# Performance work log

Measured on AMD Instinct MI355X. Metric: run time of the kernel, lower is better.

Reference implementation:

```python
import jax, jax.numpy as jnp
import numpy as np

H = 8          # attention heads
DV = 32        # per-head dim for view2global (256/8)
DS = 32        # per-head dim for scenepoint2global (256/8)
DG = 512       # n_feat_global_out
DIN = 256      # n_feat_view_in == n_feat_scenepoint_in
EPS = 1e-5


def layernorm(x, scale, bias):
    m = jnp.mean(x, axis=-1, keepdims=True)
    v = jnp.var(x, axis=-1, keepdims=True)
    return (x - m) / jnp.sqrt(v + EPS) * scale + bias


def gatv2_star(x_src, x_tgt, Wl, bl, Wr, br, att, out_bias, heads, dim):
    """GATv2Conv over a star graph: every source node -> single target node.
    x_src: [N, Din], x_tgt: [1, Din]. Returns [1, heads*dim]."""
    xl = (x_src @ Wl + bl).reshape(-1, heads, dim)          # [N,H,D] messages
    xr = (x_tgt @ Wr + br).reshape(1, heads, dim)           # [1,H,D]
    e = jax.nn.leaky_relu(xl + xr, negative_slope=0.2)      # [N,H,D]
    logits = jnp.einsum('nhd,hd->nh', e, att)               # [N,H]
    alpha = jax.nn.softmax(logits, axis=0)                  # softmax over edges per head
    out = jnp.einsum('nh,nhd->hd', alpha, xl).reshape(1, heads * dim)
    return out + out_bias


def setup_inputs() -> dict:
    key = jax.random.key(0)
    ks = jax.random.split(key, 24)
    s = 0.05
    inp = {
        'view_features': jax.random.normal(ks[0], (4096, DIN), jnp.float32),
        'scenepoint_features': jax.random.normal(ks[1], (262144, DIN), jnp.float32),
        'prev_global_features': jax.random.normal(ks[2], (1, DG), jnp.float32),
        # norm_and_proj_global2view: LayerNorm(512) -> ReLU -> Linear(512,256)
        'g2v_ln_s': jnp.ones((DG,), jnp.float32),
        'g2v_ln_b': jnp.zeros((DG,), jnp.float32),
        'g2v_W': jax.random.normal(ks[3], (DG, DIN), jnp.float32) * s,
        'g2v_b': jnp.zeros((DIN,), jnp.float32),
        # norm_and_proj_global2scenepoint
        'g2s_ln_s': jnp.ones((DG,), jnp.float32),
        'g2s_ln_b': jnp.zeros((DG,), jnp.float32),
        'g2s_W': jax.random.normal(ks[4], (DG, DIN), jnp.float32) * s,
        'g2s_b': jnp.zeros((DIN,), jnp.float32),
        # GATv2Conv view2global
        'v_Wl': jax.random.normal(ks[5], (DIN, H * DV), jnp.float32) * s,
        'v_bl': jnp.zeros((H * DV,), jnp.float32),
        'v_Wr': jax.random.normal(ks[6], (DIN, H * DV), jnp.float32) * s,
        'v_br': jnp.zeros((H * DV,), jnp.float32),
        'v_att': jax.random.normal(ks[7], (H, DV), jnp.float32) * s,
        'v_bias': jnp.zeros((H * DV,), jnp.float32),
        # GATv2Conv scenepoint2global
        's_Wl': jax.random.normal(ks[8], (DIN, H * DS), jnp.float32) * s,
        's_bl': jnp.zeros((H * DS,), jnp.float32),
        's_Wr': jax.random.normal(ks[9], (DIN, H * DS), jnp.float32) * s,
        's_br': jnp.zeros((H * DS,), jnp.float32),
        's_att': jax.random.normal(ks[10], (H, DS), jnp.float32) * s,
        's_bias': jnp.zeros((H * DS,), jnp.float32),
        # norm_pre_mlp + mlp (single Linear 512->512, no norm inside mlp)
        'pre_ln_s': jnp.ones((DG,), jnp.float32),
        'pre_ln_b': jnp.zeros((DG,), jnp.float32),
        'mlp_W': jax.random.normal(ks[11], (DG, DG), jnp.float32) * s,
        'mlp_b': jnp.zeros((DG,), jnp.float32),
    }
    return inp


def reference(view_features, scenepoint_features, prev_global_features,
              g2v_ln_s, g2v_ln_b, g2v_W, g2v_b,
              g2s_ln_s, g2s_ln_b, g2s_W, g2s_b,
              v_Wl, v_bl, v_Wr, v_br, v_att, v_bias,
              s_Wl, s_bl, s_Wr, s_br, s_att, s_bias,
              pre_ln_s, pre_ln_b, mlp_W, mlp_b):
    # target-node input features for each star graph
    xt_v = jax.nn.relu(layernorm(prev_global_features, g2v_ln_s, g2v_ln_b)) @ g2v_W + g2v_b
    xt_s = jax.nn.relu(layernorm(prev_global_features, g2s_ln_s, g2s_ln_b)) @ g2s_W + g2s_b
    v2g = gatv2_star(view_features, xt_v, v_Wl, v_bl, v_Wr, v_br, v_att, v_bias, H, DV)
    s2g = gatv2_star(scenepoint_features, xt_s, s_Wl, s_bl, s_Wr, s_br, s_att, s_bias, H, DS)
    x = jnp.concatenate([v2g, s2g], axis=1)                 # [1, 512] == n_feat_global_out
    x = prev_global_features + x                            # stateful residual
    x_skip = x
    x = jax.nn.relu(layernorm(x, pre_ln_s, pre_ln_b))       # norm_pre_mlp + relu
    x = x @ mlp_W + mlp_b                                   # mlp (0 hidden layers)
    return x_skip + x
```

## Files before the change

### kernel.cpp

```cpp
#include <hip/hip_runtime.h>
#include <hip/hip_bf16.h>

typedef unsigned short ushort_t;
typedef __attribute__((ext_vector_type(8))) short bf16x8;
typedef __attribute__((ext_vector_type(4))) float f32x4;

#define NBS 480
#define NBV 32
#define SLDS 264

#define WS_XR    0
#define WS_ACC   512
#define WS_SKIP  1040
#define WS_XN    1552

__device__ __forceinline__ float bf2f(ushort_t u) {
    union { unsigned int i; float f; } v; v.i = ((unsigned int)u) << 16; return v.f;
}
__device__ __forceinline__ ushort_t f2bf(float f) {
    union { float f; unsigned int i; } v; v.f = f;
    unsigned int x = v.i;
    return (ushort_t)((x + 0x7fffu + ((x >> 16) & 1u)) >> 16);
}
template<bool F32>
__device__ __forceinline__ float ldT(const void* p, int i) {
    if (F32) return ((const float*)p)[i];
    return bf2f(((const ushort_t*)p)[i]);
}
__device__ __forceinline__ bool is_bf16(const void* det) {
    return ((const ushort_t*)det)[0] == 0x3F80u;
}

__device__ __forceinline__ float qsum16(float x) {
    union { float f; int i; } a, b;
#define QS_STEP(CTRL) { a.f = x; b.i = __builtin_amdgcn_update_dpp(0, a.i, CTRL, 0xF, 0xF, true); x += b.f; }
    QS_STEP(0x128)
    QS_STEP(0x124)
    QS_STEP(0x122)
    QS_STEP(0x121)
#undef QS_STEP
    return x;
}

template<bool F32>
__global__ __launch_bounds__(512)
void prep_k(const void* __restrict__ prev,
            const void* __restrict__ lns_v, const void* __restrict__ lnb_v,
            const void* __restrict__ W_v,   const void* __restrict__ b_v,
            const void* __restrict__ Wr_v,  const void* __restrict__ br_v,
            const void* __restrict__ lns_s, const void* __restrict__ lnb_s,
            const void* __restrict__ W_s,   const void* __restrict__ b_s,
            const void* __restrict__ Wr_s,  const void* __restrict__ br_s,
            float* __restrict__ xr, float* __restrict__ accSO)
{
    if (is_bf16(lns_v) == F32) return;
    const int br = blockIdx.x;
    const void* lns = br ? lns_s : lns_v;
    const void* lnb = br ? lnb_s : lnb_v;
    const void* W   = br ? W_s   : W_v;
    const void* bb  = br ? b_s   : b_v;
    const void* Wr  = br ? Wr_s  : Wr_v;
    const void* brr = br ? br_s  : br_v;
    const int t = threadIdx.x;
    for (int i = t; i < 264; i += 512) accSO[br*264 + i] = 0.f;

    __shared__ float g[512];
    __shared__ float xt[256];
    __shared__ float red[16];
    __shared__ float stats[2];
    __shared__ float part[512];

    float a0 = ldT<F32>(prev, t);
    float s1 = a0, s2 = a0*a0;
#pragma unroll
    for (int s = 1; s < 64; s <<= 1) { s1 += __shfl_xor(s1, s); s2 += __shfl_xor(s2, s); }
    if ((t & 63) == 0) { red[t >> 6] = s1; red[8 + (t >> 6)] = s2; }
    __syncthreads();
    if (t == 0) {
        float a = 0.f, q = 0.f;
        for (int i = 0; i < 8; i++) { a += red[i]; q += red[8 + i]; }
        float mean = a / 512.f;
        stats[0] = mean;
        stats[1] = rsqrtf(q / 512.f - mean*mean + 1e-5f);
    }
    __syncthreads();
    g[t] = fmaxf((a0 - stats[0])*stats[1]*ldT<F32>(lns, t) + ldT<F32>(lnb, t), 0.f);
    __syncthreads();

    const int c = t & 255, kh = t >> 8;
    {
        const int base = kh * 256;
        float acc = 0.f;
#pragma unroll 8
        for (int i = 0; i < 256; i++) acc += g[base + i] * ldT<F32>(W, (base + i)*256 + c);
        part[t] = acc;
    }
    __syncthreads();
    if (t < 256) xt[t] = part[t] + part[t + 256] + ldT<F32>(bb, t);
    __syncthreads();

    {
        const int b2 = kh * 128;
        float acc2 = 0.f;
#pragma unroll 8
        for (int j = 0; j < 128; j++) acc2 += xt[b2 + j] * ldT<F32>(Wr, (b2 + j)*256 + c);
        part[t] = acc2;
    }
    __syncthreads();
    if (t < 256) xr[br*256 + t] = part[t] + part[t + 256] + ldT<F32>(brr, t);
}

template<bool F32>
__global__ __launch_bounds__(512, 2)
void gat_k(const void* __restrict__ view_x, const void* __restrict__ scene_x,
           const void* __restrict__ v_Wl, const void* __restrict__ s_Wl,
           const float* __restrict__ xr_all,
           const void* __restrict__ v_bl, const void* __restrict__ s_bl,
           const void* __restrict__ v_att, const void* __restrict__ s_att,
           const void* __restrict__ det,
           float* __restrict__ accSO)
{
    if (is_bf16(det) == F32) return;

    const int tid = threadIdx.x;
    const int wave = tid >> 6;
    const int lane = tid & 63;
    const int quad = lane >> 4;
    const int li   = lane & 15;

    const int bid = blockIdx.x;
    const bool scene = bid < NBS;
    const void* xsrc = scene ? scene_x : view_x;
    const void* Wl   = scene ? s_Wl : v_Wl;
    const float* xrp = xr_all + (scene ? 256 : 0);
    const void* blp  = scene ? s_bl  : v_bl;
    const void* attp = scene ? s_att : v_att;
    float* accR      = accSO + (scene ? 264 : 0);
    const int ntiles = scene ? 4096 : 64;
    const int nb     = scene ? NBS : NBV;
    const int slot   = scene ? bid : (bid - NBS);

    bf16x8 Bf[2][8];
#pragma unroll
    for (int nt = 0; nt < 2; nt++)
#pragma unroll
        for (int k = 0; k < 8; k++) {
            union { ushort_t u[8]; bf16x8 v; } tmp;
#pragma unroll
            for (int j = 0; j < 8; j++) {
                int idx = (k*32 + quad*8 + j)*256 + (wave*32 + nt*16 + li);
                tmp.u[j] = F32 ? f2bf(((const float*)Wl)[idx]) : ((const ushort_t*)Wl)[idx];
            }
            Bf[nt][k] = tmp.v;
        }

    const int c0 = wave*32 + li;
    const float xr0 = xrp[c0],             xr1 = xrp[c0 + 16];
    const float at0 = ldT<F32>(attp, c0),  at1 = ldT<F32>(attp, c0 + 16);
    const float bl0 = ldT<F32>(blp, c0),   bl1 = ldT<F32>(blp, c0 + 16);

    float Ssum = 0.f, oa0 = 0.f, oa1 = 0.f;

    __shared__ __align__(16) ushort_t alds[2][64 * SLDS];

    auto stage = [&](int tile, int i) -> int4 {
        int f = tid + 512*i;
        int row = f >> 5, c8 = f & 31;
        size_t base = (size_t)(tile*64 + row)*256 + c8*8;
        if (F32) {
            const float* p = (const float*)xsrc + base;
            float4 a = *(const float4*)p, b = *(const float4*)(p + 4);
            union { ushort_t u[8]; int4 v; } t_;
            t_.u[0]=f2bf(a.x); t_.u[1]=f2bf(a.y); t_.u[2]=f2bf(a.z); t_.u[3]=f2bf(a.w);
            t_.u[4]=f2bf(b.x); t_.u[5]=f2bf(b.y); t_.u[6]=f2bf(b.z); t_.u[7]=f2bf(b.w);
            return t_.v;
        }
        return *(const int4*)((const ushort_t*)xsrc + base);
    };
    auto ldsw = [&](int b, int4* src) {
#pragma unroll
        for (int i = 0; i < 4; i++) {
            int f = tid + 512*i;
            int row = f >> 5, c8 = f & 31;
            *(int4*)(&alds[b][row*SLDS + c8*8]) = src[i];
        }
    };

    int4 pf[2][4];
    {
        int4 t0[4];
#pragma unroll
        for (int i = 0; i < 4; i++) t0[i] = stage(slot, i);
        ldsw(0, t0);
        if (slot + nb < ntiles) {
#pragma unroll
            for (int i = 0; i < 4; i++) pf[0][i] = stage(slot + nb, i);
        }
        if (slot + 2*nb < ntiles) {
#pragma unroll
            for (int i = 0; i < 4; i++) pf[1][i] = stage(slot + 2*nb, i);
        }
        __syncthreads();
    }

    int buf = 0, par = 0;
    for (int t = slot; t < ntiles; t += nb) {
        f32x4 acc[4][2] = {};
#pragma unroll
        for (int k = 0; k < 8; k++) {
            bf16x8 a[4];
#pragma unroll
            for (int m = 0; m < 4; m++)
                a[m] = *(const bf16x8*)(&alds[buf][(m*16 + li)*SLDS + k*32 + quad*8]);
#pragma unroll
            for (int m = 0; m < 4; m++) {
                acc[m][0] = __builtin_amdgcn_mfma_f32_16x16x32_bf16(a[m], Bf[0][k], acc[m][0], 0, 0, 0);
                acc[m][1] = __builtin_amdgcn_mfma_f32_16x16x32_bf16(a[m], Bf[1][k], acc[m][1], 0, 0, 0);
            }
        }

#pragma unroll
        for (int m = 0; m < 4; m++) {
#pragma unroll
            for (int r = 0; r < 4; r++) {
                float x0 = acc[m][0][r] + bl0;
                float x1 = acc[m][1][r] + bl1;
                float e0 = x0 + xr0; e0 = e0 > 0.f ? e0 : 0.2f*e0;
                float e1 = x1 + xr1; e1 = e1 > 0.f ? e1 : 0.2f*e1;
                float p = qsum16(at0*e0 + at1*e1);
                float w = __expf(fminf(p, 60.f));
                Ssum += w;
                oa0 += w * x0;
                oa1 += w * x1;
            }
        }

        if (t + nb < ntiles) {
            ldsw(buf ^ 1, pf[par]);
            int tf = t + 3*nb;
            if (tf < ntiles) {
#pragma unroll
                for (int i = 0; i < 4; i++) pf[par][i] = stage(tf, i);
            }
        }
        __syncthreads();
        buf ^= 1; par ^= 1;
    }

    Ssum += __shfl_xor(Ssum, 16); Ssum += __shfl_xor(Ssum, 32);
    oa0  += __shfl_xor(oa0, 16);  oa0  += __shfl_xor(oa0, 32);
    oa1  += __shfl_xor(oa1, 16);  oa1  += __shfl_xor(oa1, 32);

    if (lane == 0) atomicAdd(&accR[wave], Ssum);
    if (lane < 16) {
        atomicAdd(&accR[8 + wave*32 + lane],      oa0);
        atomicAdd(&accR[8 + wave*32 + 16 + lane], oa1);
    }
}

template<bool F32>
__global__ __launch_bounds__(512)
void combine_k(const float* __restrict__ accSO,
               const void* __restrict__ prev,
               const void* __restrict__ v_bias, const void* __restrict__ s_bias,
               const void* __restrict__ pre_s, const void* __restrict__ pre_b,
               const void* __restrict__ det,
               float* __restrict__ x_skip, float* __restrict__ xn)
{
    if (is_bf16(det) == F32) return;
    const int t = threadIdx.x;
    const int branch = t >> 8, c = t & 255, h = c >> 5;
    float S = accSO[branch*264 + h];
    float o = accSO[branch*264 + 8 + c];
    const void* bias = branch ? s_bias : v_bias;
    float xv = ldT<F32>(prev, t) + o / S + ldT<F32>(bias, c);
    x_skip[t] = xv;
    __shared__ float red[16];
    __shared__ float stats[2];
    float s1 = xv, s2 = xv*xv;
#pragma unroll
    for (int s = 1; s < 64; s <<= 1) { s1 += __shfl_xor(s1, s); s2 += __shfl_xor(s2, s); }
    if ((t & 63) == 0) { red[t >> 6] = s1; red[8 + (t >> 6)] = s2; }
    __syncthreads();
    if (t == 0) {
        float a = 0.f, q = 0.f;
        for (int i = 0; i < 8; i++) { a += red[i]; q += red[8 + i]; }
        float mean = a / 512.f;
        stats[0] = mean;
        stats[1] = rsqrtf(q / 512.f - mean*mean + 1e-5f);
    }
    __syncthreads();
    float xnv = (xv - stats[0]) * stats[1] * ldT<F32>(pre_s, t) + ldT<F32>(pre_b, t);
    xn[t] = fmaxf(xnv, 0.f);
}

template<bool F32>
__global__ __launch_bounds__(256)
void mlp_k(const float* __restrict__ x_skip, const float* __restrict__ xn,
           const void* __restrict__ W, const void* __restrict__ mb,
           const void* __restrict__ det,
           void* __restrict__ out)
{
    if (is_bf16(det) == F32) return;
    __shared__ float xs[512];
    __shared__ float part[256];
    const int t = threadIdx.x;
    for (int i = t; i < 512; i += 256) xs[i] = xn[i];
    __syncthreads();
    const int c = blockIdx.x*128 + (t & 127);
    const int kh = t >> 7;
    const int b = kh * 256;
    float acc = 0.f;
#pragma unroll 8
    for (int i = 0; i < 256; i++) acc += xs[b + i] * ldT<F32>(W, (b + i)*512 + c);
    part[t] = acc;
    __syncthreads();
    if (t < 128) {
        float r = x_skip[c] + part[t] + part[t + 128] + ldT<F32>(mb, c);
        if (F32) ((float*)out)[c] = r;
        else     ((ushort_t*)out)[c] = f2bf(r);
    }
}

extern "C" void kernel_launch(void* const* d_in, const int* in_sizes, int n_in,
                              void* d_out, int out_size, void* d_ws, size_t ws_size,
                              hipStream_t stream)
{
    const void* view_x  = d_in[0];
    const void* scene_x = d_in[1];
    const void* prev    = d_in[2];
    const void* g2v_lns = d_in[3];
    const void* g2v_lnb = d_in[4];
    const void* g2v_W   = d_in[5];
    const void* g2v_b   = d_in[6];
    const void* g2s_lns = d_in[7];
    const void* g2s_lnb = d_in[8];
    const void* g2s_W   = d_in[9];
    const void* g2s_b   = d_in[10];
    const void* v_Wl    = d_in[11];
    const void* v_bl    = d_in[12];
    const void* v_Wr    = d_in[13];
    const void* v_br    = d_in[14];
    const void* v_att   = d_in[15];
    const void* v_bias  = d_in[16];
    const void* s_Wl    = d_in[17];
    const void* s_bl    = d_in[18];
    const void* s_Wr    = d_in[19];
    const void* s_br    = d_in[20];
    const void* s_att   = d_in[21];
    const void* s_bias  = d_in[22];
    const void* pre_s   = d_in[23];
    const void* pre_b   = d_in[24];
    const void* mlp_W   = d_in[25];
    const void* mlp_b   = d_in[26];

    float* wsf    = (float*)d_ws;
    float* xr     = wsf + WS_XR;
    float* accSO  = wsf + WS_ACC;
    float* x_skip = wsf + WS_SKIP;
    float* xn     = wsf + WS_XN;

    prep_k<false><<<dim3(2), dim3(512), 0, stream>>>(prev,
                                              g2v_lns, g2v_lnb, g2v_W, g2v_b, v_Wr, v_br,
                                              g2s_lns, g2s_lnb, g2s_W, g2s_b, s_Wr, s_br,
                                              xr, accSO);
    prep_k<true><<<dim3(2), dim3(512), 0, stream>>>(prev,
                                              g2v_lns, g2v_lnb, g2v_W, g2v_b, v_Wr, v_br,
                                              g2s_lns, g2s_lnb, g2s_W, g2s_b, s_Wr, s_br,
                                              xr, accSO);
    gat_k<false><<<dim3(NBS + NBV), dim3(512), 0, stream>>>(view_x, scene_x, v_Wl, s_Wl, xr,
                                                            v_bl, s_bl, v_att, s_att,
                                                            g2v_lns, accSO);
    gat_k<true><<<dim3(NBS + NBV), dim3(512), 0, stream>>>(view_x, scene_x, v_Wl, s_Wl, xr,
                                                           v_bl, s_bl, v_att, s_att,
                                                           g2v_lns, accSO);
    combine_k<false><<<dim3(1), dim3(512), 0, stream>>>(accSO, prev, v_bias, s_bias,
                                                        pre_s, pre_b, g2v_lns, x_skip, xn);
    combine_k<true><<<dim3(1), dim3(512), 0, stream>>>(accSO, prev, v_bias, s_bias,
                                                       pre_s, pre_b, g2v_lns, x_skip, xn);
    mlp_k<false><<<dim3(4), dim3(256), 0, stream>>>(x_skip, xn, mlp_W, mlp_b, g2v_lns, d_out);
    mlp_k<true><<<dim3(4), dim3(256), 0, stream>>>(x_skip, xn, mlp_W, mlp_b, g2v_lns, d_out);
}
```

Before: 562.5 us.

## Launch one block per tile with async LDS loads and bucketed atomics

Replaces the persistent grid-stride GAT kernel (512 blocks looping over tiles with register-prefetch double buffering) with one block per 64-row tile. In bf16 mode tiles are loaded straight into XOR-swizzled LDS using global_load_lds. Accumulation atomics are spread across 16 bucket copies to reduce contention, and combine sums the buckets. The small prep and mlp GEMVs batch 32 weight loads before accumulating, and mlp uses more blocks. The cost is that every block now reloads the full 256x256 Wl weight fragment into registers, and there are many more block launches and atomics.

```diff
diff --git a/kernel.cpp b/kernel.cpp
--- a/kernel.cpp
+++ b/kernel.cpp
@@ -5,14 +5,14 @@
 typedef __attribute__((ext_vector_type(8))) short bf16x8;
 typedef __attribute__((ext_vector_type(4))) float f32x4;
 
-#define NBS 480
-#define NBV 32
-#define SLDS 264
+#define NSCENE 4096
+#define NVIEW  64
+#define NBUCK  16
 
 #define WS_XR    0
 #define WS_ACC   512
-#define WS_SKIP  1040
-#define WS_XN    1552
+#define WS_SKIP  (512 + NBUCK*528)
+#define WS_XN    (WS_SKIP + 512)
 
 __device__ __forceinline__ float bf2f(ushort_t u) {
     union { unsigned int i; float f; } v; v.i = ((unsigned int)u) << 16; return v.f;
@@ -30,7 +30,11 @@
 __device__ __forceinline__ bool is_bf16(const void* det) {
     return ((const ushort_t*)det)[0] == 0x3F80u;
 }
-
+__device__ __forceinline__ void async16(const void* g, void* lds) {
+    __builtin_amdgcn_global_load_lds(
+        (const __attribute__((address_space(1))) unsigned int*)g,
+        (__attribute__((address_space(3))) unsigned int*)lds, 16, 0, 0);
+}
 __device__ __forceinline__ float qsum16(float x) {
     union { float f; int i; } a, b;
 #define QS_STEP(CTRL) { a.f = x; b.i = __builtin_amdgcn_update_dpp(0, a.i, CTRL, 0xF, 0xF, true); x += b.f; }
@@ -62,7 +66,9 @@
     const void* Wr  = br ? Wr_s  : Wr_v;
     const void* brr = br ? br_s  : br_v;
     const int t = threadIdx.x;
-    for (int i = t; i < 264; i += 512) accSO[br*264 + i] = 0.f;
+#pragma unroll
+    for (int b = 0; b < NBUCK; b++)
+        for (int i = t; i < 264; i += 512) accSO[b*528 + br*264 + i] = 0.f;
 
     __shared__ float g[512];
     __shared__ float xt[256];
@@ -91,19 +97,28 @@
     {
         const int base = kh * 256;
         float acc = 0.f;
-#pragma unroll 8
-        for (int i = 0; i < 256; i++) acc += g[base + i] * ldT<F32>(W, (base + i)*256 + c);
+        for (int ii = 0; ii < 256; ii += 32) {
+            float wv[32];
+#pragma unroll
+            for (int u = 0; u < 32; u++) wv[u] = ldT<F32>(W, (base + ii + u)*256 + c);
+#pragma unroll
+            for (int u = 0; u < 32; u++) acc += g[base + ii + u] * wv[u];
+        }
         part[t] = acc;
     }
     __syncthreads();
     if (t < 256) xt[t] = part[t] + part[t + 256] + ldT<F32>(bb, t);
     __syncthreads();
-
     {
         const int b2 = kh * 128;
         float acc2 = 0.f;
-#pragma unroll 8
-        for (int j = 0; j < 128; j++) acc2 += xt[b2 + j] * ldT<F32>(Wr, (b2 + j)*256 + c);
+        for (int ii = 0; ii < 128; ii += 32) {
+            float wv[32];
+#pragma unroll
+            for (int u = 0; u < 32; u++) wv[u] = ldT<F32>(Wr, (b2 + ii + u)*256 + c);
+#pragma unroll
+            for (int u = 0; u < 32; u++) acc2 += xt[b2 + ii + u] * wv[u];
+        }
         part[t] = acc2;
     }
     __syncthreads();
@@ -122,23 +137,44 @@
 {
     if (is_bf16(det) == F32) return;
 
-    const int tid = threadIdx.x;
+    const int tid  = threadIdx.x;
     const int wave = tid >> 6;
     const int lane = tid & 63;
     const int quad = lane >> 4;
     const int li   = lane & 15;
 
-    const int bid = blockIdx.x;
-    const bool scene = bid < NBS;
+    const int bid   = blockIdx.x;
+    const bool scene = bid < NSCENE;
     const void* xsrc = scene ? scene_x : view_x;
     const void* Wl   = scene ? s_Wl : v_Wl;
     const float* xrp = xr_all + (scene ? 256 : 0);
     const void* blp  = scene ? s_bl  : v_bl;
     const void* attp = scene ? s_att : v_att;
-    float* accR      = accSO + (scene ? 264 : 0);
-    const int ntiles = scene ? 4096 : 64;
-    const int nb     = scene ? NBS : NBV;
-    const int slot   = scene ? bid : (bid - NBS);
+    float* accR      = accSO + (bid & (NBUCK - 1))*528 + (scene ? 264 : 0);
+    const int tile   = scene ? bid : (bid - NSCENE);
+
+    __shared__ __align__(16) ushort_t alds[64 * 256];
+
+    {
+        const int l5 = lane >> 5, g2 = lane & 31;
+#pragma unroll
+        for (int j = 0; j < 4; j++) {
+            const int ci  = wave*4 + j;
+            const int row = 2*ci + l5;
+            const int g   = (g2 & 24) | ((g2 & 7) ^ (row & 7));
+            const size_t gelem = (size_t)(tile*64 + row)*256 + g*8;
+            if (F32) {
+                const float* p = (const float*)xsrc + gelem;
+                float4 a = *(const float4*)p, b = *(const float4*)(p + 4);
+                union { ushort_t u[8]; int4 v; } t_;
+                t_.u[0]=f2bf(a.x); t_.u[1]=f2bf(a.y); t_.u[2]=f2bf(a.z); t_.u[3]=f2bf(a.w);
+                t_.u[4]=f2bf(b.x); t_.u[5]=f2bf(b.y); t_.u[6]=f2bf(b.z); t_.u[7]=f2bf(b.w);
+                *(int4*)(&alds[ci*512 + lane*8]) = t_.v;
+            } else {
+                async16((const ushort_t*)xsrc + gelem, &alds[ci*512]);
+            }
+        }
+    }
 
     bf16x8 Bf[2][8];
 #pragma unroll
@@ -155,96 +191,45 @@
         }
 
     const int c0 = wave*32 + li;
-    const float xr0 = xrp[c0],             xr1 = xrp[c0 + 16];
-    const float at0 = ldT<F32>(attp, c0),  at1 = ldT<F32>(attp, c0 + 16);
-    const float bl0 = ldT<F32>(blp, c0),   bl1 = ldT<F32>(blp, c0 + 16);
+    const float xr0 = xrp[c0],            xr1 = xrp[c0 + 16];
+    const float at0 = ldT<F32>(attp, c0), at1 = ldT<F32>(attp, c0 + 16);
+    const float bl0 = ldT<F32>(blp, c0),  bl1 = ldT<F32>(blp, c0 + 16);
+
+    __syncthreads();
+
+    f32x4 acc[4][2] = {};
+#pragma unroll
+    for (int k = 0; k < 8; k++) {
+        bf16x8 a[4];
+#pragma unroll
+        for (int m = 0; m < 4; m++) {
+            const int r  = m*16 + li;
+            const int gq = k*4 + quad;
+            const int gp = (gq & 24) | ((gq & 7) ^ (li & 7));
+            a[m] = *(const bf16x8*)(&alds[r*256 + gp*8]);
+        }
+#pragma unroll
+        for (int m = 0; m < 4; m++) {
+            acc[m][0] = __builtin_amdgcn_mfma_f32_16x16x32_bf16(a[m], Bf[0][k], acc[m][0], 0, 0, 0);
+            acc[m][1] = __builtin_amdgcn_mfma_f32_16x16x32_bf16(a[m], Bf[1][k], acc[m][1], 0, 0, 0);
+        }
+    }
 
     float Ssum = 0.f, oa0 = 0.f, oa1 = 0.f;
-
-    __shared__ __align__(16) ushort_t alds[2][64 * SLDS];
-
-    auto stage = [&](int tile, int i) -> int4 {
-        int f = tid + 512*i;
-        int row = f >> 5, c8 = f & 31;
-        size_t base = (size_t)(tile*64 + row)*256 + c8*8;
-        if (F32) {
-            const float* p = (const float*)xsrc + base;
-            float4 a = *(const float4*)p, b = *(const float4*)(p + 4);
-            union { ushort_t u[8]; int4 v; } t_;
-            t_.u[0]=f2bf(a.x); t_.u[1]=f2bf(a.y); t_.u[2]=f2bf(a.z); t_.u[3]=f2bf(a.w);
-            t_.u[4]=f2bf(b.x); t_.u[5]=f2bf(b.y); t_.u[6]=f2bf(b.z); t_.u[7]=f2bf(b.w);
-            return t_.v;
-        }
-        return *(const int4*)((const ushort_t*)xsrc + base);
-    };
-    auto ldsw = [&](int b, int4* src) {
-#pragma unroll
-        for (int i = 0; i < 4; i++) {
-            int f = tid + 512*i;
-            int row = f >> 5, c8 = f & 31;
-            *(int4*)(&alds[b][row*SLDS + c8*8]) = src[i];
-        }
-    };
-
-    int4 pf[2][4];
-    {
-        int4 t0[4];
-#pragma unroll
-        for (int i = 0; i < 4; i++) t0[i] = stage(slot, i);
-        ldsw(0, t0);
-        if (slot + nb < ntiles) {
-#pragma unroll
-            for (int i = 0; i < 4; i++) pf[0][i] = stage(slot + nb, i);
-        }
-        if (slot + 2*nb < ntiles) {
-#pragma unroll
-            for (int i = 0; i < 4; i++) pf[1][i] = stage(slot + 2*nb, i);
-        }
-        __syncthreads();
-    }
-
-    int buf = 0, par = 0;
-    for (int t = slot; t < ntiles; t += nb) {
-        f32x4 acc[4][2] = {};
-#pragma unroll
-        for (int k = 0; k < 8; k++) {
-            bf16x8 a[4];
-#pragma unroll
-            for (int m = 0; m < 4; m++)
-                a[m] = *(const bf16x8*)(&alds[buf][(m*16 + li)*SLDS + k*32 + quad*8]);
-#pragma unroll
-            for (int m = 0; m < 4; m++) {
-                acc[m][0] = __builtin_amdgcn_mfma_f32_16x16x32_bf16(a[m], Bf[0][k], acc[m][0], 0, 0, 0);
-                acc[m][1] = __builtin_amdgcn_mfma_f32_16x16x32_bf16(a[m], Bf[1][k], acc[m][1], 0, 0, 0);
-            }
-        }
-
-#pragma unroll
-        for (int m = 0; m < 4; m++) {
-#pragma unroll
-            for (int r = 0; r < 4; r++) {
-                float x0 = acc[m][0][r] + bl0;
-                float x1 = acc[m][1][r] + bl1;
-                float e0 = x0 + xr0; e0 = e0 > 0.f ? e0 : 0.2f*e0;
-                float e1 = x1 + xr1; e1 = e1 > 0.f ? e1 : 0.2f*e1;
-                float p = qsum16(at0*e0 + at1*e1);
-                float w = __expf(fminf(p, 60.f));
-                Ssum += w;
-                oa0 += w * x0;
-                oa1 += w * x1;
-            }
-        }
-
-        if (t + nb < ntiles) {
-            ldsw(buf ^ 1, pf[par]);
-            int tf = t + 3*nb;
-            if (tf < ntiles) {
-#pragma unroll
-                for (int i = 0; i < 4; i++) pf[par][i] = stage(tf, i);
-            }
-        }
-        __syncthreads();
-        buf ^= 1; par ^= 1;
+#pragma unroll
+    for (int m = 0; m < 4; m++) {
+#pragma unroll
+        for (int r = 0; r < 4; r++) {
+            float x0 = acc[m][0][r] + bl0;
+            float x1 = acc[m][1][r] + bl1;
+            float e0 = x0 + xr0; e0 = e0 > 0.f ? e0 : 0.2f*e0;
+            float e1 = x1 + xr1; e1 = e1 > 0.f ? e1 : 0.2f*e1;
+            float p = qsum16(at0*e0 + at1*e1);
+            float w = __expf(fminf(p, 60.f));
+            Ssum += w;
+            oa0 += w * x0;
+            oa1 += w * x1;
+        }
     }
 
     Ssum += __shfl_xor(Ssum, 16); Ssum += __shfl_xor(Ssum, 32);
@@ -270,8 +255,12 @@
     if (is_bf16(det) == F32) return;
     const int t = threadIdx.x;
     const int branch = t >> 8, c = t & 255, h = c >> 5;
-    float S = accSO[branch*264 + h];
-    float o = accSO[branch*264 + 8 + c];
+    float S = 0.f, o = 0.f;
+#pragma unroll
+    for (int b = 0; b < NBUCK; b++) {
+        S += accSO[b*528 + branch*264 + h];
+        o += accSO[b*528 + branch*264 + 8 + c];
+    }
     const void* bias = branch ? s_bias : v_bias;
     float xv = ldT<F32>(prev, t) + o / S + ldT<F32>(bias, c);
     x_skip[t] = xv;
@@ -307,16 +296,22 @@
     const int t = threadIdx.x;
     for (int i = t; i < 512; i += 256) xs[i] = xn[i];
     __syncthreads();
-    const int c = blockIdx.x*128 + (t & 127);
-    const int kh = t >> 7;
-    const int b = kh * 256;
+    const int c  = blockIdx.x*64 + (t & 63);
+    const int kh = t >> 6;
+    const int b  = kh * 128;
     float acc = 0.f;
-#pragma unroll 8
-    for (int i = 0; i < 256; i++) acc += xs[b + i] * ldT<F32>(W, (b + i)*512 + c);
+    for (int ii = 0; ii < 128; ii += 32) {
+        float wv[32];
+#pragma unroll
+        for (int u = 0; u < 32; u++) wv[u] = ldT<F32>(W, (b + ii + u)*512 + c);
+#pragma unroll
+        for (int u = 0; u < 32; u++) acc += xs[b + ii + u] * wv[u];
+    }
     part[t] = acc;
     __syncthreads();
-    if (t < 128) {
-        float r = x_skip[c] + part[t] + part[t + 128] + ldT<F32>(mb, c);
+    if (t < 64) {
+        float r = x_skip[c] + part[t] + part[t + 64] + part[t + 128] + part[t + 192]
+                + ldT<F32>(mb, c);
         if (F32) ((float*)out)[c] = r;
         else     ((ushort_t*)out)[c] = f2bf(r);
     }
@@ -368,16 +363,16 @@
                                               g2v_lns, g2v_lnb, g2v_W, g2v_b, v_Wr, v_br,
                                               g2s_lns, g2s_lnb, g2s_W, g2s_b, s_Wr, s_br,
                                               xr, accSO);
-    gat_k<false><<<dim3(NBS + NBV), dim3(512), 0, stream>>>(view_x, scene_x, v_Wl, s_Wl, xr,
-                                                            v_bl, s_bl, v_att, s_att,
-                                                            g2v_lns, accSO);
-    gat_k<true><<<dim3(NBS + NBV), dim3(512), 0, stream>>>(view_x, scene_x, v_Wl, s_Wl, xr,
-                                                           v_bl, s_bl, v_att, s_att,
-                                                           g2v_lns, accSO);
+    gat_k<false><<<dim3(NSCENE + NVIEW), dim3(512), 0, stream>>>(view_x, scene_x, v_Wl, s_Wl,
+                                                                 xr, v_bl, s_bl, v_att, s_att,
+                                                                 g2v_lns, accSO);
+    gat_k<true><<<dim3(NSCENE + NVIEW), dim3(512), 0, stream>>>(view_x, scene_x, v_Wl, s_Wl,
+                                                                xr, v_bl, s_bl, v_att, s_att,
+                                                                g2v_lns, accSO);
     combine_k<false><<<dim3(1), dim3(512), 0, stream>>>(accSO, prev, v_bias, s_bias,
                                                         pre_s, pre_b, g2v_lns, x_skip, xn);
     combine_k<true><<<dim3(1), dim3(512), 0, stream>>>(accSO, prev, v_bias, s_bias,
                                                        pre_s, pre_b, g2v_lns, x_skip, xn);
-    mlp_k<false><<<dim3(4), dim3(256), 0, stream>>>(x_skip, xn, mlp_W, mlp_b, g2v_lns, d_out);
-    mlp_k<true><<<dim3(4), dim3(256), 0, stream>>>(x_skip, xn, mlp_W, mlp_b, g2v_lns, d_out);
-}
+    mlp_k<false><<<dim3(8), dim3(256), 0, stream>>>(x_skip, xn, mlp_W, mlp_b, g2v_lns, d_out);
+    mlp_k<true><<<dim3(8), dim3(256), 0, stream>>>(x_skip, xn, mlp_W, mlp_b, g2v_lns, d_out);
+}
```

New measurement: 505.4 us. -10.1%, faster.
